# Kernel tuning notes

Measured on AMD Instinct MI355X. Metric: run time of the kernel, lower is better.

## Reference

```python
import jax, jax.numpy as jnp
import numpy as np

DEPTH = 10                      # levels per complete binary tree (node_order in [0, DEPTH-1])
N_TREES = 512
NODES_PER_TREE = 2 ** DEPTH - 1  # 1023
N_FEAT = 64
N_HIDDEN = 64


def _build_forest():
    """Forest of N_TREES complete binary trees, heap-indexed within each tree.

    node_order: 0 at leaves, DEPTH-1 at root (pytorch-tree-lstm convention).
    adjacency_list: (parent, child) pairs, parents grouped consecutively.
    edge_order: node_order of the parent of each edge.
    """
    npt = NODES_PER_TREE
    idx = np.arange(npt)
    level = np.floor(np.log2(idx + 1)).astype(np.int64)   # 0 at root
    order = (DEPTH - 1) - level                            # 0 at leaves
    internal = idx[2 * idx + 2 < npt]
    parents = np.repeat(internal, 2)
    children = np.empty_like(parents)
    children[0::2] = 2 * internal + 1
    children[1::2] = 2 * internal + 2
    base_adj = np.stack([parents, children], axis=1)       # [e, 2]
    eorder = order[parents]
    off = (np.arange(N_TREES) * npt).astype(np.int64)
    node_order = np.tile(order, N_TREES)
    adj = (base_adj[None, :, :] + off[:, None, None]).reshape(-1, 2)
    edge_order = np.tile(eorder, N_TREES)
    return node_order, adj, edge_order


def setup_inputs() -> dict:
    key = jax.random.key(0)
    ks = jax.random.split(key, 10)
    node_order, adj, edge_order = _build_forest()
    N = N_TREES * NODES_PER_TREE
    H, F = N_HIDDEN, N_FEAT
    s_in = 1.0 / np.sqrt(F)
    s_h = 1.0 / np.sqrt(H)
    return {
        "features": jax.random.normal(ks[0], (N, F), jnp.float32),
        "node_order": jnp.asarray(node_order),
        "adjacency_list": jnp.asarray(adj),
        "edge_order": jnp.asarray(edge_order),
        "w_iou": jax.random.normal(ks[1], (3 * H, F), jnp.float32) * s_in,
        "b_iou": jnp.zeros((3 * H,), jnp.float32),
        "u_iou": jax.random.normal(ks[2], (3 * H, H), jnp.float32) * s_h,
        "w_f": jax.random.normal(ks[3], (H, F), jnp.float32) * s_in,
        "b_f": jnp.zeros((H,), jnp.float32),
        "u_f": jax.random.normal(ks[4], (H, H), jnp.float32) * s_h,
        "lin0_w": jax.random.normal(ks[5], (H, H), jnp.float32) * s_h,
        "lin0_b": jnp.zeros((H,), jnp.float32),
        "lin1_w": jax.random.normal(ks[6], (H, H), jnp.float32) * s_h,
        "lin1_b": jnp.zeros((H,), jnp.float32),
        "out_w": jax.random.normal(ks[7], (1, H), jnp.float32) * s_h,
        "out_b": jnp.zeros((1,), jnp.float32),
    }


def _tree_lstm(features, node_order, parent, child, edge_order,
               w_iou, b_iou, u_iou, w_f, b_f, u_f):
    N = features.shape[0]
    H = u_f.shape[0]
    # input contributions are level-independent: compute once for all nodes
    iou_x = features @ w_iou.T + b_iou   # [N, 3H]
    f_x = features @ w_f.T + b_f         # [N, H]
    h = jnp.zeros((N, H), features.dtype)
    c = jnp.zeros((N, H), features.dtype)
    for n in range(DEPTH):               # dependency-chained level sweep
        nmask = (node_order == n)[:, None]
        emask = (edge_order == n)[:, None].astype(features.dtype)
        child_h = h[child]               # [E, H] gather
        child_c = c[child]
        # sum of children h per parent, restricted to this level's edges
        h_sum = jax.ops.segment_sum(child_h * emask, parent, num_segments=N)
        iou = iou_x + h_sum @ u_iou.T
        i, o, u = jnp.split(iou, 3, axis=1)
        i = jax.nn.sigmoid(i)
        o = jax.nn.sigmoid(o)
        u = jnp.tanh(u)
        # per-edge forget gates; contributions masked to this level's edges
        f = jax.nn.sigmoid(f_x[parent] + child_h @ u_f.T)
        c_sum = jax.ops.segment_sum(f * child_c * emask, parent, num_segments=N)
        c = jnp.where(nmask, i * u + c_sum, c)
        h = jnp.where(nmask, o * jnp.tanh(c), h)
    return h, c


def reference(features, node_order, adjacency_list, edge_order,
              w_iou, b_iou, u_iou, w_f, b_f, u_f,
              lin0_w, lin0_b, lin1_w, lin1_b, out_w, out_b):
    parent = adjacency_list[:, 0]
    child = adjacency_list[:, 1]
    h, _ = _tree_lstm(features, node_order, parent, child, edge_order,
                      w_iou, b_iou, u_iou, w_f, b_f, u_f)
    # unbatch + mean pool per tree (all trees have equal size -> reshape)
    x = h.reshape(N_TREES, NODES_PER_TREE, -1).mean(axis=1)
    x = jax.nn.relu(x)                   # dropout is identity in eval mode
    x = jax.nn.relu(x @ lin0_w.T + lin0_b)
    x = jax.nn.relu(x @ lin1_w.T + lin1_b)
    return (x @ out_w.T + out_b).ravel()  # [N_TREES]
```

## Files before the change

### kernel.cpp

```cpp
#include <hip/hip_runtime.h>
#include <math.h>

#define NTREES 512
#define DEPTH  10
#define NPT    1023
#define NTOT   (NTREES * NPT)
#define H      64
#define PART_SLOTS 32256

typedef __attribute__((ext_vector_type(8))) short bf16x8;
typedef __attribute__((ext_vector_type(4))) float f32x4;

__device__ __forceinline__ float sigm(float x)  { return __builtin_amdgcn_rcpf(1.0f + __expf(-x)); }
__device__ __forceinline__ float ftanh(float x) { return fmaf(-2.0f, __builtin_amdgcn_rcpf(__expf(2.0f * x) + 1.0f), 1.0f); }

__device__ __forceinline__ unsigned short bf_hi(float f) {
    unsigned u = __float_as_uint(f);
    return (unsigned short)((u + 0x7fffu + ((u >> 16) & 1u)) >> 16);
}
__device__ __forceinline__ float bf_f(unsigned short h) {
    return __uint_as_float(((unsigned)h) << 16);
}
__device__ __forceinline__ void split8(const float v[8], bf16x8& hi, bf16x8& lo) {
    #pragma unroll
    for (int e = 0; e < 8; ++e) {
        unsigned short hh = bf_hi(v[e]);
        hi[e] = (short)hh;
        lo[e] = (short)bf_hi(v[e] - bf_f(hh));
    }
}

#define MFMA(a, b, c) __builtin_amdgcn_mfma_f32_16x16x32_bf16((a), (b), (c), 0, 0, 0)

__device__ __forceinline__ void gl_lds16(const void* g, void* s) {
    __builtin_amdgcn_global_load_lds(
        (const __attribute__((address_space(1))) unsigned*)g,
        (__attribute__((address_space(3))) unsigned*)s, 16, 0, 0);
}

__global__ void prep_b(const float* __restrict__ w_iou, const float* __restrict__ u_iou,
                       const float* __restrict__ w_f,  const float* __restrict__ u_f,
                       unsigned short* __restrict__ B)
{
    int idx  = blockIdx.x * 256 + threadIdx.x;
    int unit = idx >> 3;
    int e    = idx & 7;
    int l    = unit & 63;
    float v;
    int hl;
    if (unit < 6144) {
        int sp = (unit >= 3072) ? 1 : 0;
        int r  = unit - sp * 3072;
        int q  = r >> 6;
        hl     = q & 1;
        int ts = q >> 1;
        int s_ = ts & 1;
        int t  = ts >> 1;
        int s  = sp * 2 + s_;
        int col = t * 16 + (l & 15);
        int k   = 32 * s + 8 * (l >> 4) + e;
        v = (k < 64) ? w_iou[col * H + k] : u_iou[col * H + (k - 64)];
    } else {
        int r  = unit - 6144;
        int q  = r >> 6;
        hl     = q & 1;
        int xu = (q >> 1) & 1;
        int ts = q >> 2;
        int s  = ts & 1;
        int t  = ts >> 1;
        int col = t * 16 + (l & 15);
        int k   = 32 * s + 8 * (l >> 4) + e;
        v = xu ? u_f[col * H + k] : w_f[col * H + k];
    }
    unsigned short hv = bf_hi(v);
    B[idx] = hl ? bf_hi(v - bf_f(hv)) : hv;
}

__device__ __forceinline__ void store_partial(float psum[4], int l, int wid,
                                              float* __restrict__ partw)
{
    #pragma unroll
    for (int t = 0; t < 4; ++t) {
        float v = psum[t];
        v += __shfl_xor(v, 16);
        v += __shfl_xor(v, 32);
        if (l < 16) partw[(size_t)wid * H + 16 * t + l] = v;
    }
}

__global__ __launch_bounds__(256, 3)
void leaf_mfma(const float* __restrict__ feat, const unsigned short* __restrict__ Braw,
               const float* __restrict__ b_iou,
               float* __restrict__ h, float* __restrict__ c,
               float* __restrict__ partw, int do_part)
{
    __shared__ bf16x8 Bs[3072];
    int tid = threadIdx.x;
    int l   = tid & 63;
    int w   = tid >> 6;
    int base = blockIdx.x * 64 + w * 16;
    int g    = base + (l & 15);
    int nrow = (g >> 9) * NPT + 511 + (g & 511);
    int ko   = 8 * (l >> 4);

    const float* fb = feat + (size_t)nrow * H + ko;
    float4 fr0 = *(const float4*)(fb);
    float4 fr1 = *(const float4*)(fb + 4);
    float4 fr2 = *(const float4*)(fb + 32);
    float4 fr3 = *(const float4*)(fb + 36);

    const bf16x8* Bg = (const bf16x8*)Braw;
    for (int u = tid; u < 3072; u += 256) gl_lds16(Bg + u, Bs + u);
    __syncthreads();

    bf16x8 fh[2], fl[2];
    { float v[8] = {fr0.x,fr0.y,fr0.z,fr0.w,fr1.x,fr1.y,fr1.z,fr1.w}; split8(v, fh[0], fl[0]); }
    { float v[8] = {fr2.x,fr2.y,fr2.z,fr2.w,fr3.x,fr3.y,fr3.z,fr3.w}; split8(v, fh[1], fl[1]); }

    f32x4 acc[12];
    #pragma unroll
    for (int t = 0; t < 12; ++t) acc[t] = (f32x4){0.f,0.f,0.f,0.f};
    __builtin_amdgcn_s_setprio(1);
    #pragma unroll
    for (int t = 0; t < 12; ++t) {
        #pragma unroll
        for (int s = 0; s < 2; ++s) {
            bf16x8 bh = Bs[((t * 2 + s) * 2 + 0) * 64 + l];
            bf16x8 bl = Bs[((t * 2 + s) * 2 + 1) * 64 + l];
            acc[t] = MFMA(fh[s], bh, acc[t]);
            acc[t] = MFMA(fh[s], bl, acc[t]);
            acc[t] = MFMA(fl[s], bh, acc[t]);
        }
    }
    __builtin_amdgcn_s_setprio(0);
    int colb = l & 15;
    float psum[4] = {0.f, 0.f, 0.f, 0.f};
    #pragma unroll
    for (int r = 0; r < 4; ++r) {
        int gr = base + (l >> 4) * 4 + r;
        int nr = (gr >> 9) * NPT + 511 + (gr & 511);
        #pragma unroll
        for (int t = 0; t < 4; ++t) {
            int j = 16 * t + colb;
            float ai = acc[t][r]     + b_iou[j];
            float ao = acc[4 + t][r] + b_iou[64 + j];
            float au = acc[8 + t][r] + b_iou[128 + j];
            float cv = sigm(ai) * ftanh(au);
            float hval = sigm(ao) * ftanh(cv);
            c[(size_t)nr * H + j] = cv;
            h[(size_t)nr * H + j] = hval;
            psum[t] += hval;
        }
    }
    if (do_part) store_partial(psum, l, blockIdx.x * 4 + w, partw);
}

__global__ __launch_bounds__(256, 3)
void internal_mfma(const float* __restrict__ feat, const unsigned short* __restrict__ Braw,
                   const float* __restrict__ b_iou, const float* __restrict__ b_f,
                   float* __restrict__ h, float* __restrict__ c, int lvl,
                   float* __restrict__ partw, int woff)
{
    __shared__ bf16x8 Bs[3072];
    int tid = threadIdx.x;
    int l   = tid & 63;
    int w   = tid >> 6;
    int m   = 1 << lvl;
    int base  = blockIdx.x * 64 + w * 16;
    int g     = base + (l & 15);
    int tree  = g >> lvl, i = g & (m - 1);
    int local = (m - 1) + i;
    int nrow  = tree * NPT + local;
    int crow0 = tree * NPT + 2 * local + 1;
    int ko    = 8 * (l >> 4);
    int colb  = l & 15;

    const float* fb  = feat + (size_t)nrow * H + ko;
    float4 fr0 = *(const float4*)(fb);
    float4 fr1 = *(const float4*)(fb + 4);
    float4 fr2 = *(const float4*)(fb + 32);
    float4 fr3 = *(const float4*)(fb + 36);
    const float* h0b = h + (size_t)crow0 * H + ko;
    const float* h1b = h0b + H;
    float4 a00 = *(const float4*)(h0b);
    float4 a01 = *(const float4*)(h0b + 4);
    float4 a02 = *(const float4*)(h0b + 32);
    float4 a03 = *(const float4*)(h0b + 36);
    float4 a10 = *(const float4*)(h1b);
    float4 a11 = *(const float4*)(h1b + 4);
    float4 a12 = *(const float4*)(h1b + 32);
    float4 a13 = *(const float4*)(h1b + 36);

    const bf16x8* Bg = (const bf16x8*)Braw;
    for (int u = tid; u < 2048; u += 256) gl_lds16(Bg + 6144 + u, Bs + u);
    __syncthreads();

    bf16x8 fh[2], fl[2], sh[2], sl[2], zh[2], zl[2];
    { float v[8] = {fr0.x,fr0.y,fr0.z,fr0.w,fr1.x,fr1.y,fr1.z,fr1.w}; split8(v, fh[0], fl[0]); }
    { float v[8] = {fr2.x,fr2.y,fr2.z,fr2.w,fr3.x,fr3.y,fr3.z,fr3.w}; split8(v, fh[1], fl[1]); }
    {
        float v0[8] = {a00.x,a00.y,a00.z,a00.w,a01.x,a01.y,a01.z,a01.w};
        float v1[8] = {a10.x,a10.y,a10.z,a10.w,a11.x,a11.y,a11.z,a11.w};
        float vs[8];
        #pragma unroll
        for (int e = 0; e < 8; ++e) vs[e] = v0[e] + v1[e];
        split8(v0, zh[0], zl[0]); split8(vs, sh[0], sl[0]);
    }
    {
        float v0[8] = {a02.x,a02.y,a02.z,a02.w,a03.x,a03.y,a03.z,a03.w};
        float v1[8] = {a12.x,a12.y,a12.z,a12.w,a13.x,a13.y,a13.z,a13.w};
        float vs[8];
        #pragma unroll
        for (int e = 0; e < 8; ++e) vs[e] = v0[e] + v1[e];
        split8(v0, zh[1], zl[1]); split8(vs, sh[1], sl[1]);
    }

    float f0[4][4], f1[4][4];
    __builtin_amdgcn_s_setprio(1);
    #pragma unroll
    for (int t = 0; t < 4; ++t) {
        f32x4 ax  = (f32x4){0.f,0.f,0.f,0.f};
        f32x4 as_ = (f32x4){0.f,0.f,0.f,0.f};
        f32x4 az  = (f32x4){0.f,0.f,0.f,0.f};
        #pragma unroll
        for (int s = 0; s < 2; ++s) {
            int qb = (t * 2 + s) * 4;
            bf16x8 bxh = Bs[(qb + 0) * 64 + l];
            bf16x8 bxl = Bs[(qb + 1) * 64 + l];
            bf16x8 buh = Bs[(qb + 2) * 64 + l];
            bf16x8 bul = Bs[(qb + 3) * 64 + l];
            ax  = MFMA(fh[s], bxh, ax);  ax  = MFMA(fh[s], bxl, ax);  ax  = MFMA(fl[s], bxh, ax);
            as_ = MFMA(sh[s], buh, as_); as_ = MFMA(sh[s], bul, as_); as_ = MFMA(sl[s], buh, as_);
            az  = MFMA(zh[s], buh, az);  az  = MFMA(zh[s], bul, az);  az  = MFMA(zl[s], buh, az);
        }
        #pragma unroll
        for (int r = 0; r < 4; ++r) {
            float afx = ax[r] + b_f[16 * t + colb];
            f0[t][r] = sigm(afx + az[r]);
            f1[t][r] = sigm(afx + (as_[r] - az[r]));
        }
    }
    __builtin_amdgcn_s_setprio(0);
    __syncthreads();

    for (int u = tid; u < 3072; u += 256) gl_lds16(Bg + u, Bs + u);
    __syncthreads();
    f32x4 acc[12];
    #pragma unroll
    for (int t = 0; t < 12; ++t) acc[t] = (f32x4){0.f,0.f,0.f,0.f};
    __builtin_amdgcn_s_setprio(1);
    #pragma unroll
    for (int t = 0; t < 12; ++t) {
        #pragma unroll
        for (int s = 0; s < 2; ++s) {
            bf16x8 bh = Bs[((t * 2 + s) * 2 + 0) * 64 + l];
            bf16x8 bl = Bs[((t * 2 + s) * 2 + 1) * 64 + l];
            acc[t] = MFMA(fh[s], bh, acc[t]);
            acc[t] = MFMA(fh[s], bl, acc[t]);
            acc[t] = MFMA(fl[s], bh, acc[t]);
        }
    }
    __builtin_amdgcn_s_setprio(0);
    __syncthreads();

    for (int u = tid; u < 3072; u += 256) gl_lds16(Bg + 3072 + u, Bs + u);
    __syncthreads();
    __builtin_amdgcn_s_setprio(1);
    #pragma unroll
    for (int t = 0; t < 12; ++t) {
        #pragma unroll
        for (int s = 0; s < 2; ++s) {
            bf16x8 bh = Bs[((t * 2 + s) * 2 + 0) * 64 + l];
            bf16x8 bl = Bs[((t * 2 + s) * 2 + 1) * 64 + l];
            acc[t] = MFMA(sh[s], bh, acc[t]);
            acc[t] = MFMA(sh[s], bl, acc[t]);
            acc[t] = MFMA(sl[s], bh, acc[t]);
        }
    }
    __builtin_amdgcn_s_setprio(0);

    float psum[4] = {0.f, 0.f, 0.f, 0.f};
    #pragma unroll
    for (int r = 0; r < 4; ++r) {
        int gr = base + (l >> 4) * 4 + r;
        int treer = gr >> lvl, ir = gr & (m - 1);
        int lr = (m - 1) + ir;
        int nr = treer * NPT + lr;
        size_t ch0 = (size_t)(treer * NPT + 2 * lr + 1) * H;
        size_t ch1 = ch0 + H;
        #pragma unroll
        for (int t = 0; t < 4; ++t) {
            int j = 16 * t + colb;
            float ai = acc[t][r]     + b_iou[j];
            float ao = acc[4 + t][r] + b_iou[64 + j];
            float au = acc[8 + t][r] + b_iou[128 + j];
            float cv = sigm(ai) * ftanh(au) + f0[t][r] * c[ch0 + j] + f1[t][r] * c[ch1 + j];
            float hval = sigm(ao) * ftanh(cv);
            c[(size_t)nr * H + j] = cv;
            h[(size_t)nr * H + j] = hval;
            psum[t] += hval;
        }
    }
    if (woff >= 0) store_partial(psum, l, woff + blockIdx.x * 4 + w, partw);
}

__global__ __launch_bounds__(512)
void small_levels(const float* __restrict__ feat, const unsigned short* __restrict__ Braw,
                  const float* __restrict__ b_iou, const float* __restrict__ b_f,
                  float* __restrict__ h, float* __restrict__ c)
{
    extern __shared__ bf16x8 Bs[];
    const bf16x8* Bg = (const bf16x8*)Braw;
    int tid = threadIdx.x;
    for (int u = tid; u < 8192; u += 512) gl_lds16(Bg + u, Bs + u);
    __syncthreads();

    int l    = tid & 63;
    int w    = tid >> 6;
    int colb = l & 15;
    int ko   = 8 * (l >> 4);

    for (int lvl = 3; lvl >= 0; --lvl) {
        if (w < (1 << lvl)) {
            int m     = 1 << lvl;
            int base  = blockIdx.x * (16 << lvl) + w * 16;
            int g     = base + colb;
            int tree  = g >> lvl, i = g & (m - 1);
            int local = (m - 1) + i;
            int nrow  = tree * NPT + local;
            int crow0 = tree * NPT + 2 * local + 1;

            const float* fb  = feat + (size_t)nrow * H + ko;
            float4 fr0 = *(const float4*)(fb);
            float4 fr1 = *(const float4*)(fb + 4);
            float4 fr2 = *(const float4*)(fb + 32);
            float4 fr3 = *(const float4*)(fb + 36);
            const float* h0b = h + (size_t)crow0 * H + ko;
            const float* h1b = h0b + H;
            float4 a00 = *(const float4*)(h0b);
            float4 a01 = *(const float4*)(h0b + 4);
            float4 a02 = *(const float4*)(h0b + 32);
            float4 a03 = *(const float4*)(h0b + 36);
            float4 a10 = *(const float4*)(h1b);
            float4 a11 = *(const float4*)(h1b + 4);
            float4 a12 = *(const float4*)(h1b + 32);
            float4 a13 = *(const float4*)(h1b + 36);

            bf16x8 fh[2], fl[2], sh[2], sl[2], zh[2], zl[2];
            { float v[8] = {fr0.x,fr0.y,fr0.z,fr0.w,fr1.x,fr1.y,fr1.z,fr1.w}; split8(v, fh[0], fl[0]); }
            { float v[8] = {fr2.x,fr2.y,fr2.z,fr2.w,fr3.x,fr3.y,fr3.z,fr3.w}; split8(v, fh[1], fl[1]); }
            {
                float v0[8] = {a00.x,a00.y,a00.z,a00.w,a01.x,a01.y,a01.z,a01.w};
                float v1[8] = {a10.x,a10.y,a10.z,a10.w,a11.x,a11.y,a11.z,a11.w};
                float vs[8];
                #pragma unroll
                for (int e = 0; e < 8; ++e) vs[e] = v0[e] + v1[e];
                split8(v0, zh[0], zl[0]); split8(vs, sh[0], sl[0]);
            }
            {
                float v0[8] = {a02.x,a02.y,a02.z,a02.w,a03.x,a03.y,a03.z,a03.w};
                float v1[8] = {a12.x,a12.y,a12.z,a12.w,a13.x,a13.y,a13.z,a13.w};
                float vs[8];
                #pragma unroll
                for (int e = 0; e < 8; ++e) vs[e] = v0[e] + v1[e];
                split8(v0, zh[1], zl[1]); split8(vs, sh[1], sl[1]);
            }

            float f0[4][4], f1[4][4];
            #pragma unroll
            for (int t = 0; t < 4; ++t) {
                f32x4 ax  = (f32x4){0.f,0.f,0.f,0.f};
                f32x4 as_ = (f32x4){0.f,0.f,0.f,0.f};
                f32x4 az  = (f32x4){0.f,0.f,0.f,0.f};
                #pragma unroll
                for (int s = 0; s < 2; ++s) {
                    int qb = (t * 2 + s) * 4;
                    bf16x8 bxh = Bs[6144 + (qb + 0) * 64 + l];
                    bf16x8 bxl = Bs[6144 + (qb + 1) * 64 + l];
                    bf16x8 buh = Bs[6144 + (qb + 2) * 64 + l];
                    bf16x8 bul = Bs[6144 + (qb + 3) * 64 + l];
                    ax  = MFMA(fh[s], bxh, ax);  ax  = MFMA(fh[s], bxl, ax);  ax  = MFMA(fl[s], bxh, ax);
                    as_ = MFMA(sh[s], buh, as_); as_ = MFMA(sh[s], bul, as_); as_ = MFMA(sl[s], buh, as_);
                    az  = MFMA(zh[s], buh, az);  az  = MFMA(zh[s], bul, az);  az  = MFMA(zl[s], buh, az);
                }
                #pragma unroll
                for (int r = 0; r < 4; ++r) {
                    float afx = ax[r] + b_f[16 * t + colb];
                    f0[t][r] = sigm(afx + az[r]);
                    f1[t][r] = sigm(afx + (as_[r] - az[r]));
                }
            }

            f32x4 acc[12];
            #pragma unroll
            for (int t = 0; t < 12; ++t) acc[t] = (f32x4){0.f,0.f,0.f,0.f};
            #pragma unroll
            for (int t = 0; t < 12; ++t) {
                #pragma unroll
                for (int s = 0; s < 2; ++s) {
                    bf16x8 bh = Bs[((t * 2 + s) * 2 + 0) * 64 + l];
                    bf16x8 bl = Bs[((t * 2 + s) * 2 + 1) * 64 + l];
                    acc[t] = MFMA(fh[s], bh, acc[t]);
                    acc[t] = MFMA(fh[s], bl, acc[t]);
                    acc[t] = MFMA(fl[s], bh, acc[t]);
                }
            }
            #pragma unroll
            for (int t = 0; t < 12; ++t) {
                #pragma unroll
                for (int s = 0; s < 2; ++s) {
                    bf16x8 bh = Bs[3072 + ((t * 2 + s) * 2 + 0) * 64 + l];
                    bf16x8 bl = Bs[3072 + ((t * 2 + s) * 2 + 1) * 64 + l];
                    acc[t] = MFMA(sh[s], bh, acc[t]);
                    acc[t] = MFMA(sh[s], bl, acc[t]);
                    acc[t] = MFMA(sl[s], bh, acc[t]);
                }
            }

            #pragma unroll
            for (int r = 0; r < 4; ++r) {
                int gr = base + (l >> 4) * 4 + r;
                int treer = gr >> lvl, ir = gr & (m - 1);
                int lr = (m - 1) + ir;
                int nr = treer * NPT + lr;
                size_t ch0 = (size_t)(treer * NPT + 2 * lr + 1) * H;
                size_t ch1 = ch0 + H;
                #pragma unroll
                for (int t = 0; t < 4; ++t) {
                    int j = 16 * t + colb;
                    float ai = acc[t][r]     + b_iou[j];
                    float ao = acc[4 + t][r] + b_iou[64 + j];
                    float au = acc[8 + t][r] + b_iou[128 + j];
                    float cv = sigm(ai) * ftanh(au) + f0[t][r] * c[ch0 + j] + f1[t][r] * c[ch1 + j];
                    float hval = sigm(ao) * ftanh(cv);
                    c[(size_t)nr * H + j] = cv;
                    h[(size_t)nr * H + j] = hval;
                }
            }
        }
        __syncthreads();
    }
}

__global__ __launch_bounds__(64)
void final_mlp(const float* __restrict__ h, const float* __restrict__ partw,
               const float* __restrict__ l0w, const float* __restrict__ l0b,
               const float* __restrict__ l1w, const float* __restrict__ l1b,
               const float* __restrict__ ow,  const float* __restrict__ ob,
               float* __restrict__ out)
{
    int tree = blockIdx.x;
    int f = threadIdx.x;
    float s = 0.0f;
    #pragma unroll 4
    for (int k = 0; k < 32; ++k) s += partw[(size_t)(tree * 32 + k) * H + f];
    #pragma unroll 4
    for (int k = 0; k < 16; ++k) s += partw[(size_t)(16384 + tree * 16 + k) * H + f];
    #pragma unroll
    for (int k = 0; k < 8; ++k)  s += partw[(size_t)(24576 + tree * 8 + k) * H + f];
    #pragma unroll
    for (int k = 0; k < 4; ++k)  s += partw[(size_t)(28672 + tree * 4 + k) * H + f];
    #pragma unroll
    for (int k = 0; k < 2; ++k)  s += partw[(size_t)(30720 + tree * 2 + k) * H + f];
    s += partw[(size_t)(31744 + tree) * H + f];
    const float* hb = h + (size_t)tree * NPT * H;
    #pragma unroll
    for (int i = 0; i < 15; ++i) s += hb[i * H + f];
    float x = fmaxf(s * (1.0f / 1023.0f), 0.0f);

    __shared__ float xb[H];
    __shared__ float yb[H];
    xb[f] = x;
    __syncthreads();
    float acc = l0b[f];
    #pragma unroll
    for (int k = 0; k < H; ++k) acc = fmaf(l0w[f * H + k], xb[k], acc);
    acc = fmaxf(acc, 0.0f);
    yb[f] = acc;
    __syncthreads();
    float acc2 = l1b[f];
    #pragma unroll
    for (int k = 0; k < H; ++k) acc2 = fmaf(l1w[f * H + k], yb[k], acc2);
    acc2 = fmaxf(acc2, 0.0f);
    float t = ow[f] * acc2;
    #pragma unroll
    for (int off = 32; off > 0; off >>= 1) t += __shfl_down(t, off);
    if (f == 0) out[tree] = t + ob[0];
}

__global__ __launch_bounds__(256)
void pool_kernel(const float* __restrict__ h, float* __restrict__ x)
{
    __shared__ float red[4][H];
    int tree = blockIdx.x;
    int f = threadIdx.x & 63;
    int seg = threadIdx.x >> 6;
    const float* basep = h + (size_t)tree * NPT * H;
    int i0 = seg * 256, i1 = i0 + 256; if (i1 > NPT) i1 = NPT;
    float s = 0.f;
    for (int i = i0; i < i1; ++i) s += basep[i * H + f];
    red[seg][f] = s;
    __syncthreads();
    if (seg == 0) {
        float tot = red[0][f] + red[1][f] + red[2][f] + red[3][f];
        x[tree * H + f] = fmaxf(tot * (1.0f / 1023.0f), 0.0f);
    }
}

__global__ __launch_bounds__(64)
void mlp_kernel(const float* __restrict__ x,
                const float* __restrict__ l0w, const float* __restrict__ l0b,
                const float* __restrict__ l1w, const float* __restrict__ l1b,
                const float* __restrict__ ow,  const float* __restrict__ ob,
                float* __restrict__ out)
{
    int tree = blockIdx.x;
    int j = threadIdx.x;
    __shared__ float xb[H];
    __shared__ float yb[H];
    xb[j] = x[tree * H + j];
    __syncthreads();
    float acc = l0b[j];
    #pragma unroll
    for (int k = 0; k < H; ++k) acc = fmaf(l0w[j * H + k], xb[k], acc);
    acc = fmaxf(acc, 0.0f);
    yb[j] = acc;
    __syncthreads();
    float acc2 = l1b[j];
    #pragma unroll
    for (int k = 0; k < H; ++k) acc2 = fmaf(l1w[j * H + k], yb[k], acc2);
    acc2 = fmaxf(acc2, 0.0f);
    float t = ow[j] * acc2;
    #pragma unroll
    for (int off = 32; off > 0; off >>= 1) t += __shfl_down(t, off);
    if (j == 0) out[tree] = t + ob[0];
}

extern "C" void kernel_launch(void* const* d_in, const int* in_sizes, int n_in,
                              void* d_out, int out_size, void* d_ws, size_t ws_size,
                              hipStream_t stream)
{
    const float* feat  = (const float*)d_in[0];
    const float* w_iou = (const float*)d_in[4];
    const float* b_iou = (const float*)d_in[5];
    const float* u_iou = (const float*)d_in[6];
    const float* w_f   = (const float*)d_in[7];
    const float* b_f   = (const float*)d_in[8];
    const float* u_f   = (const float*)d_in[9];
    const float* l0w   = (const float*)d_in[10];
    const float* l0b   = (const float*)d_in[11];
    const float* l1w   = (const float*)d_in[12];
    const float* l1b   = (const float*)d_in[13];
    const float* ow    = (const float*)d_in[14];
    const float* ob    = (const float*)d_in[15];
    float* out = (float*)d_out;

    float* h = (float*)d_ws;
    float* c = h + (size_t)NTOT * H;
    float* x = c + (size_t)NTOT * H;
    unsigned short* Bf = (unsigned short*)(x + NTREES * H);
    float* partw = (float*)(Bf + 65536);
    size_t needed = (size_t)((char*)(partw + (size_t)PART_SLOTS * H) - (char*)d_ws);
    int use_part = (ws_size >= needed) ? 1 : 0;

    hipFuncSetAttribute(reinterpret_cast<const void*>(small_levels),
                        hipFuncAttributeMaxDynamicSharedMemorySize, 131072);

    prep_b<<<256, 256, 0, stream>>>(w_iou, u_iou, w_f, u_f, Bf);
    leaf_mfma<<<4096, 256, 0, stream>>>(feat, Bf, b_iou, h, c, partw, use_part);
    for (int lvl = DEPTH - 2; lvl >= 4; --lvl) {
        int woff = (use_part) ? (32768 - (64 << lvl)) : -1;
        internal_mfma<<<8 << lvl, 256, 0, stream>>>(
            feat, Bf, b_iou, b_f, h, c, lvl, partw, woff);
    }
    small_levels<<<32, 512, 131072, stream>>>(feat, Bf, b_iou, b_f, h, c);
    if (use_part) {
        final_mlp<<<NTREES, 64, 0, stream>>>(h, partw, l0w, l0b, l1w, l1b, ow, ob, out);
    } else {
        pool_kernel<<<NTREES, 256, 0, stream>>>(h, x);
        mlp_kernel<<<NTREES, 64, 0, stream>>>(x, l0w, l0b, l1w, l1b, ow, ob, out);
    }
}
```

Measured before the change: 268.1 us.

## Double-buffer LDS weight loads in halves to overlap with MFMA compute

Splits each weight-matrix stage into two 1536-entry halves of the LDS buffer. The next half's global-to-LDS copy is issued while MFMAs consume the other half, so the load latency before each GEMM phase is partly hidden. The forget-gate weights are reorganised so the W_f and U_f parts land in separate halves. This adds more barriers and relies on async copy completion ordering at each sync.

Measured after the change: 270.8 us. About the same (+1.0%).

```diff
diff --git a/kernel.cpp b/kernel.cpp
--- a/kernel.cpp
+++ b/kernel.cpp
@@ -110,8 +110,9 @@
     float4 fr3 = *(const float4*)(fb + 36);
 
     const bf16x8* Bg = (const bf16x8*)Braw;
-    for (int u = tid; u < 3072; u += 256) gl_lds16(Bg + u, Bs + u);
-    __syncthreads();
+    for (int u = tid; u < 1536; u += 256) gl_lds16(Bg + u, Bs + u);
+    __syncthreads();
+    for (int u = tid; u < 1536; u += 256) gl_lds16(Bg + 1536 + u, Bs + 1536 + u);
 
     bf16x8 fh[2], fl[2];
     { float v[8] = {fr0.x,fr0.y,fr0.z,fr0.w,fr1.x,fr1.y,fr1.z,fr1.w}; split8(v, fh[0], fl[0]); }
@@ -122,7 +123,7 @@
     for (int t = 0; t < 12; ++t) acc[t] = (f32x4){0.f,0.f,0.f,0.f};
     __builtin_amdgcn_s_setprio(1);
     #pragma unroll
-    for (int t = 0; t < 12; ++t) {
+    for (int t = 0; t < 6; ++t) {
         #pragma unroll
         for (int s = 0; s < 2; ++s) {
             bf16x8 bh = Bs[((t * 2 + s) * 2 + 0) * 64 + l];
@@ -133,6 +134,22 @@
         }
     }
     __builtin_amdgcn_s_setprio(0);
+    __syncthreads();
+    __builtin_amdgcn_s_setprio(1);
+    #pragma unroll
+    for (int t = 6; t < 12; ++t) {
+        int tt = t - 6;
+        #pragma unroll
+        for (int s = 0; s < 2; ++s) {
+            bf16x8 bh = Bs[1536 + ((tt * 2 + s) * 2 + 0) * 64 + l];
+            bf16x8 bl = Bs[1536 + ((tt * 2 + s) * 2 + 1) * 64 + l];
+            acc[t] = MFMA(fh[s], bh, acc[t]);
+            acc[t] = MFMA(fh[s], bl, acc[t]);
+            acc[t] = MFMA(fl[s], bh, acc[t]);
+        }
+    }
+    __builtin_amdgcn_s_setprio(0);
+
     int colb = l & 15;
     float psum[4] = {0.f, 0.f, 0.f, 0.f};
     #pragma unroll
@@ -192,8 +209,15 @@
     float4 a13 = *(const float4*)(h1b + 36);
 
     const bf16x8* Bg = (const bf16x8*)Braw;
-    for (int u = tid; u < 2048; u += 256) gl_lds16(Bg + 6144 + u, Bs + u);
-    __syncthreads();
+    for (int u = tid; u < 1024; u += 256) {
+        int q = u >> 6, li = u & 63;
+        gl_lds16(Bg + 6144 + ((q >> 1) * 4 + (q & 1)) * 64 + li, Bs + u);
+    }
+    __syncthreads();
+    for (int u = tid; u < 1024; u += 256) {
+        int q = u >> 6, li = u & 63;
+        gl_lds16(Bg + 6144 + ((q >> 1) * 4 + 2 + (q & 1)) * 64 + li, Bs + 1536 + u);
+    }
 
     bf16x8 fh[2], fl[2], sh[2], sl[2], zh[2], zl[2];
     { float v[8] = {fr0.x,fr0.y,fr0.z,fr0.w,fr1.x,fr1.y,fr1.z,fr1.w}; split8(v, fh[0], fl[0]); }
@@ -215,42 +239,54 @@
         split8(v0, zh[1], zl[1]); split8(vs, sh[1], sl[1]);
     }
 
+    f32x4 axs[4];
+    __builtin_amdgcn_s_setprio(1);
+    #pragma unroll
+    for (int t = 0; t < 4; ++t) {
+        f32x4 ax = (f32x4){0.f,0.f,0.f,0.f};
+        #pragma unroll
+        for (int s = 0; s < 2; ++s) {
+            bf16x8 bxh = Bs[((t * 2 + s) * 2 + 0) * 64 + l];
+            bf16x8 bxl = Bs[((t * 2 + s) * 2 + 1) * 64 + l];
+            ax = MFMA(fh[s], bxh, ax);  ax = MFMA(fh[s], bxl, ax);  ax = MFMA(fl[s], bxh, ax);
+        }
+        axs[t] = ax;
+    }
+    __builtin_amdgcn_s_setprio(0);
+    __syncthreads();
+    for (int u = tid; u < 1536; u += 256) gl_lds16(Bg + u, Bs + u);
+
     float f0[4][4], f1[4][4];
     __builtin_amdgcn_s_setprio(1);
     #pragma unroll
     for (int t = 0; t < 4; ++t) {
-        f32x4 ax  = (f32x4){0.f,0.f,0.f,0.f};
         f32x4 as_ = (f32x4){0.f,0.f,0.f,0.f};
         f32x4 az  = (f32x4){0.f,0.f,0.f,0.f};
         #pragma unroll
         for (int s = 0; s < 2; ++s) {
-            int qb = (t * 2 + s) * 4;
-            bf16x8 bxh = Bs[(qb + 0) * 64 + l];
-            bf16x8 bxl = Bs[(qb + 1) * 64 + l];
-            bf16x8 buh = Bs[(qb + 2) * 64 + l];
-            bf16x8 bul = Bs[(qb + 3) * 64 + l];
-            ax  = MFMA(fh[s], bxh, ax);  ax  = MFMA(fh[s], bxl, ax);  ax  = MFMA(fl[s], bxh, ax);
+            bf16x8 buh = Bs[1536 + ((t * 2 + s) * 2 + 0) * 64 + l];
+            bf16x8 bul = Bs[1536 + ((t * 2 + s) * 2 + 1) * 64 + l];
             as_ = MFMA(sh[s], buh, as_); as_ = MFMA(sh[s], bul, as_); as_ = MFMA(sl[s], buh, as_);
             az  = MFMA(zh[s], buh, az);  az  = MFMA(zh[s], bul, az);  az  = MFMA(zl[s], buh, az);
         }
         #pragma unroll
         for (int r = 0; r < 4; ++r) {
-            float afx = ax[r] + b_f[16 * t + colb];
+            float afx = axs[t][r] + b_f[16 * t + colb];
             f0[t][r] = sigm(afx + az[r]);
             f1[t][r] = sigm(afx + (as_[r] - az[r]));
         }
     }
     __builtin_amdgcn_s_setprio(0);
     __syncthreads();
-
-    for (int u = tid; u < 3072; u += 256) gl_lds16(Bg + u, Bs + u);
-    __syncthreads();
+    for (int u = tid; u < 1536; u += 256) gl_lds16(Bg + 1536 + u, Bs + 1536 + u);
+
     f32x4 acc[12];
     #pragma unroll
     for (int t = 0; t < 12; ++t) acc[t] = (f32x4){0.f,0.f,0.f,0.f};
-    __builtin_amdgcn_s_setprio(1);
-    #pragma unroll
-    for (int t = 0; t < 12; ++t) {
+
+    __builtin_amdgcn_s_setprio(1);
+    #pragma unroll
+    for (int t = 0; t < 6; ++t) {
         #pragma unroll
         for (int s = 0; s < 2; ++s) {
             bf16x8 bh = Bs[((t * 2 + s) * 2 + 0) * 64 + l];
@@ -262,16 +298,48 @@
     }
     __builtin_amdgcn_s_setprio(0);
     __syncthreads();
-
-    for (int u = tid; u < 3072; u += 256) gl_lds16(Bg + 3072 + u, Bs + u);
-    __syncthreads();
-    __builtin_amdgcn_s_setprio(1);
-    #pragma unroll
-    for (int t = 0; t < 12; ++t) {
+    for (int u = tid; u < 1536; u += 256) gl_lds16(Bg + 3072 + u, Bs + u);
+
+    __builtin_amdgcn_s_setprio(1);
+    #pragma unroll
+    for (int t = 6; t < 12; ++t) {
+        int tt = t - 6;
+        #pragma unroll
+        for (int s = 0; s < 2; ++s) {
+            bf16x8 bh = Bs[1536 + ((tt * 2 + s) * 2 + 0) * 64 + l];
+            bf16x8 bl = Bs[1536 + ((tt * 2 + s) * 2 + 1) * 64 + l];
+            acc[t] = MFMA(fh[s], bh, acc[t]);
+            acc[t] = MFMA(fh[s], bl, acc[t]);
+            acc[t] = MFMA(fl[s], bh, acc[t]);
+        }
+    }
+    __builtin_amdgcn_s_setprio(0);
+    __syncthreads();
+    for (int u = tid; u < 1536; u += 256) gl_lds16(Bg + 4608 + u, Bs + 1536 + u);
+
+    __builtin_amdgcn_s_setprio(1);
+    #pragma unroll
+    for (int t = 0; t < 6; ++t) {
         #pragma unroll
         for (int s = 0; s < 2; ++s) {
             bf16x8 bh = Bs[((t * 2 + s) * 2 + 0) * 64 + l];
             bf16x8 bl = Bs[((t * 2 + s) * 2 + 1) * 64 + l];
+            acc[t] = MFMA(sh[s], bh, acc[t]);
+            acc[t] = MFMA(sh[s], bl, acc[t]);
+            acc[t] = MFMA(sl[s], bh, acc[t]);
+        }
+    }
+    __builtin_amdgcn_s_setprio(0);
+    __syncthreads();
+
+    __builtin_amdgcn_s_setprio(1);
+    #pragma unroll
+    for (int t = 6; t < 12; ++t) {
+        int tt = t - 6;
+        #pragma unroll
+        for (int s = 0; s < 2; ++s) {
+            bf16x8 bh = Bs[1536 + ((tt * 2 + s) * 2 + 0) * 64 + l];
+            bf16x8 bl = Bs[1536 + ((tt * 2 + s) * 2 + 1) * 64 + l];
             acc[t] = MFMA(sh[s], bh, acc[t]);
             acc[t] = MFMA(sh[s], bl, acc[t]);
             acc[t] = MFMA(sl[s], bh, acc[t]);
```
